# Kernel tuning notes

Hardware: AMD Instinct MI355X
Metric: run time of the kernel (lower is better)

Reference implementation:

```python
import jax, jax.numpy as jnp
import numpy as np

N, E, D, L, R, G, NRXN = 100000, 400000, 256, 3, 4, 2000, 10


def setup_inputs() -> dict:
    key = jax.random.key(0)
    ks = jax.random.split(key, 12)
    s = 1.0 / np.sqrt(D).astype(np.float32)
    return {
        "node_feature": jax.random.normal(ks[0], (N, D), jnp.float32),
        "flag_W": jax.random.normal(ks[1], (2, D), jnp.float32) * s,
        "flag_b": jax.random.normal(ks[2], (D,), jnp.float32) * s,
        "W_self": jax.random.normal(ks[3], (L, D, D), jnp.float32) * s,
        "b_self": jax.random.normal(ks[4], (L, D), jnp.float32) * s,
        "W_rel": jax.random.normal(ks[5], (L, R, D, D), jnp.float32) * s,
        "edge_src": jax.random.randint(ks[6], (E,), 0, N, jnp.int32),
        "edge_dst": jax.random.randint(ks[7], (E,), 0, N, jnp.int32),
        "edge_type": jax.random.randint(ks[8], (E,), 0, R, jnp.int32),
        "batch": jnp.sort(jax.random.randint(ks[9], (N,), 0, G, jnp.int32)),
        "reaction": jax.random.randint(ks[10], (G,), 0, NRXN, jnp.int32),
        "center_mask": jax.random.randint(ks[11], (N,), 0, 2, jnp.int32).astype(bool),
    }


def _rgcn_layer(x, Wself, bself, Wrel, edge_src, edge_dst, edge_type, deg):
    # Relation-wise transform on all nodes [R, N, D], then per-edge gather by
    # (edge_type, src). Masks over edge_type partition edges, so overwriting
    # messages[mask] per relation == selecting the relation's transform per edge.
    h = jnp.einsum('nd,rde->rne', x, Wrel)
    messages = h[edge_type, edge_src]                         # [E, D]
    agg = jax.ops.segment_sum(messages, edge_dst, num_segments=x.shape[0]) / deg
    return jax.nn.relu(x @ Wself + bself + agg)


def reference(node_feature, flag_W, flag_b, W_self, b_self, W_rel,
              edge_src, edge_dst, edge_type, batch, reaction, center_mask):
    n = node_feature.shape[0]
    # flags = [zeros, center_mask]; node_input = node_feature + flag_linear(flags)
    flags = jnp.stack([jnp.zeros((n,), jnp.float32),
                       center_mask.astype(jnp.float32)], axis=-1)  # [N, 2]
    x = node_feature + flags @ flag_W + flag_b
    # degree normalization over destinations (same every layer), clamp min 1
    deg = jnp.maximum(
        jax.ops.segment_sum(jnp.ones((edge_dst.shape[0],), jnp.float32),
                            edge_dst, num_segments=n), 1.0)[:, None]
    hiddens = []
    for l in range(L):
        x = _rgcn_layer(x, W_self[l], b_self[l], W_rel[l],
                        edge_src, edge_dst, edge_type, deg)
        hiddens.append(x)
    node_enc = jnp.concatenate(hiddens, axis=-1)              # [N, L*D]
    # segment mean over graphs
    gsum = jax.ops.segment_sum(node_enc, batch, num_segments=G)
    gcnt = jnp.maximum(
        jax.ops.segment_sum(jnp.ones((n,), jnp.float32), batch, num_segments=G),
        1.0)[:, None]
    graph_feature = gsum / gcnt                               # [G, L*D]
    rxn = jax.nn.one_hot(reaction, NRXN, dtype=jnp.float32)   # [G, NRXN]
    graph_context = jnp.concatenate([graph_feature, rxn], axis=-1)
    node_context = jnp.concatenate(
        [node_enc, node_feature, graph_context[batch]], axis=-1)  # [N, 1802]
    return node_context, graph_context
```

## Files before the change

### kernel.cpp

```cpp
#include <hip/hip_runtime.h>
#include <hip/hip_bf16.h>

typedef _Float16 f16x8 __attribute__((ext_vector_type(8)));
typedef float f32x4 __attribute__((ext_vector_type(4)));

namespace {
constexpr int N_ = 100000;
constexpr int E_ = 400000;
constexpr int D_ = 256;
constexpr int L_ = 3;
constexpr int R_ = 4;
constexpr int G_ = 2000;
constexpr int NRXN_ = 10;
constexpr int CTXW = L_*D_ + D_ + L_*D_ + NRXN_;
constexpr int GCTXW = L_*D_ + NRXN_;
constexpr int NKT = (R_+1)*D_/32;
constexpr int NR = N_*R_;
constexpr int NB2 = (NR + 2047)/2048;
}


__global__ void k_zero(int* __restrict__ p, int n) {
  int i = blockIdx.x*256 + threadIdx.x;
  if (i < n) p[i] = 0;
}

__global__ void k_detect(const unsigned char* __restrict__ cm, int* __restrict__ meta) {
  int tid = threadIdx.x;
  int ok_i = 1, ok_f = 1;
  for (int i = tid; i < 4096; i += 256) {
    unsigned b = cm[i];
    int m = i & 3;
    if (m == 0)      { if (b > 1) ok_i = 0; if (b != 0) ok_f = 0; }
    else if (m == 1) { if (b) { ok_i = 0; ok_f = 0; } }
    else if (m == 2) { if (b) ok_i = 0; if (b != 0 && b != 0x80) ok_f = 0; }
    else             { if (b) ok_i = 0; if (b != 0 && b != 0x3f) ok_f = 0; }
  }
  int all_i = __syncthreads_and(ok_i);
  int all_f = __syncthreads_and(ok_f);
  if (tid == 0) meta[0] = all_i ? 0 : (all_f ? 1 : 2);
}

__global__ void k_hist2(const int* __restrict__ dst, const int* __restrict__ typ,
                        int* __restrict__ hist, int n) {
  int i = blockIdx.x*256 + threadIdx.x;
  if (i < n) atomicAdd(&hist[dst[i]*4 + typ[i]], 1);
}

__global__ void k_hist(const int* __restrict__ key, int* __restrict__ hist, int n) {
  int i = blockIdx.x*256 + threadIdx.x;
  if (i < n) atomicAdd(&hist[key[i]], 1);
}

__global__ void k_scan1(const int* __restrict__ h, int* __restrict__ out,
                        int* __restrict__ bsum, int n) {
  __shared__ int sh[256];
  int t = threadIdx.x;
  int base = blockIdx.x*2048 + t*8;
  int v[8]; int s = 0;
  #pragma unroll
  for (int j = 0; j < 8; ++j) { v[j] = (base+j < n) ? h[base+j] : 0; s += v[j]; }
  sh[t] = s; __syncthreads();
  for (int off = 1; off < 256; off <<= 1) {
    int x = (t >= off) ? sh[t-off] : 0;
    __syncthreads();
    sh[t] += x;
    __syncthreads();
  }
  int ex = sh[t] - s;
  #pragma unroll
  for (int j = 0; j < 8; ++j) { if (base+j < n) out[base+j] = ex; ex += v[j]; }
  if (t == 255) bsum[blockIdx.x] = sh[255];
}

__global__ void k_scan2(int* __restrict__ b, int nb) {
  __shared__ int sh[256];
  int t = threadIdx.x;
  int s = (t < nb) ? b[t] : 0;
  sh[t] = s; __syncthreads();
  for (int off = 1; off < 256; off <<= 1) {
    int x = (t >= off) ? sh[t-off] : 0;
    __syncthreads();
    sh[t] += x;
    __syncthreads();
  }
  if (t < nb) b[t] = sh[t] - s;
}

__global__ void k_scan3(int* __restrict__ eoff, const int* __restrict__ bsum,
                        int* __restrict__ cursor, int n, int total) {
  int i = blockIdx.x*256 + threadIdx.x;
  if (i < n) {
    int v = eoff[i] + bsum[i >> 11];
    eoff[i] = v;
    cursor[i] = v;
  }
  if (i == 0) eoff[n] = total;
}

__global__ void k_scatter2(const int* __restrict__ src, const int* __restrict__ dst,
                           const int* __restrict__ typ, int* __restrict__ cursor,
                           int* __restrict__ out, int n) {
  int i = blockIdx.x*256 + threadIdx.x;
  if (i < n) {
    int key = dst[i]*4 + typ[i];
    int p = atomicAdd(&cursor[key], 1);
    out[p] = src[i];
  }
}

__global__ void k_scan_small(const int* __restrict__ gh, int* __restrict__ goff, int g) {
  __shared__ int sh[256];
  int t = threadIdx.x;
  int v[8]; int s = 0;
  #pragma unroll
  for (int j = 0; j < 8; ++j) { int idx = t*8+j; v[j] = (idx < g) ? gh[idx] : 0; s += v[j]; }
  sh[t] = s; __syncthreads();
  for (int off = 1; off < 256; off <<= 1) {
    int x = (t >= off) ? sh[t-off] : 0;
    __syncthreads();
    sh[t] += x;
    __syncthreads();
  }
  int ex = sh[t] - s;
  #pragma unroll
  for (int j = 0; j < 8; ++j) { int idx = t*8+j; if (idx < g) goff[idx] = ex; ex += v[j]; }
  if (t == 255) goff[g] = sh[255];
}

__global__ void k_pack_w(const float* __restrict__ Wrel, const float* __restrict__ Wself,
                         f16x8* __restrict__ Bp) {
  int id = blockIdx.x*256 + threadIdx.x;
  if (id >= L_*NKT*16*64) return;
  int lane = id & 63; int rest = id >> 6;
  int ct = rest & 15; rest >>= 4;
  int kt = rest % NKT; int l = rest / NKT;
  int q = lane >> 4, ln = lane & 15;
  int col = ct*16 + ln;
  f16x8 o;
  #pragma unroll
  for (int j = 0; j < 8; ++j) {
    int k = kt*32 + q*8 + j;
    float v = (k < R_*D_) ? Wrel[((size_t)l*R_*D_ + k)*D_ + col]
                          : Wself[((size_t)l*D_ + (k - R_*D_))*D_ + col];
    o[j] = (_Float16)v;
  }
  Bp[id] = o;
}

__global__ void k_node_init(const float* __restrict__ nf, const float* __restrict__ fW,
                            const float* __restrict__ fb, const void* __restrict__ cm,
                            const int* __restrict__ meta, _Float16* __restrict__ xa,
                            float* __restrict__ out) {
  int n = blockIdx.x, c = threadIdx.x;
  float v = nf[(size_t)n*D_ + c];
  out[(size_t)n*CTXW + 768 + c] = v;
  int mode = meta[0];
  bool mk;
  if (mode == 0)      mk = ((const int*)cm)[n] != 0;
  else if (mode == 1) mk = ((const float*)cm)[n] != 0.f;
  else                mk = ((const unsigned char*)cm)[n] != 0;
  float x0 = v + (mk ? fW[D_ + c] : 0.f) + fb[c];
  xa[(size_t)n*D_ + c] = (_Float16)x0;
}

__global__ __launch_bounds__(256, 3)
void k_layer(const _Float16* __restrict__ xin, const f16x8* __restrict__ Bp,
             const float* __restrict__ bias, const int* __restrict__ eoff2,
             const int* __restrict__ es, float* __restrict__ outp,
             _Float16* __restrict__ xout) {
  __shared__ f16x8 As16[2][32*32];
  const int tid = threadIdx.x;
  const int lane = tid & 63, wave = tid >> 6;
  const int q = lane >> 4, ln = lane & 15;
  const int m0 = blockIdx.x * 32;
  const int kch = lane & 7;
  const int row = wave*8 + (lane >> 3);
  const int nd  = m0 + row;

  int oo[5];
  #pragma unroll
  for (int j = 0; j < 5; ++j) oo[j] = eoff2[nd*4 + j];
  const int degt = oo[4] - oo[0];
  const float invd = 1.0f / (float)(degt > 1 ? degt : 1);

  f32x4 acc[2][4];
  #pragma unroll
  for (int rt = 0; rt < 2; ++rt)
    #pragma unroll
    for (int cc = 0; cc < 4; ++cc)
      acc[rt][cc] = f32x4{0.f,0.f,0.f,0.f};

  {
    const _Float16* r0 = xin + (size_t)(m0 + ln)*D_;
    const _Float16* r1 = xin + (size_t)(m0 + 16 + ln)*D_;
    #pragma unroll
    for (int kt = 0; kt < 8; ++kt) {
      f16x8 a0 = *(const f16x8*)(r0 + kt*32 + q*8);
      f16x8 a1 = *(const f16x8*)(r1 + kt*32 + q*8);
      f16x8 b[4];
      #pragma unroll
      for (int cc = 0; cc < 4; ++cc)
        b[cc] = Bp[(size_t)((32 + kt)*16 + wave*4 + cc)*64 + lane];
      #pragma unroll
      for (int cc = 0; cc < 4; ++cc) {
        acc[0][cc] = __builtin_amdgcn_mfma_f32_16x16x32_f16(a0, b[cc], acc[0][cc], 0,0,0);
        acc[1][cc] = __builtin_amdgcn_mfma_f32_16x16x32_f16(a1, b[cc], acc[1][cc], 0,0,0);
      }
    }
  }

  #pragma unroll
  for (int r = 0; r < R_; ++r) {
    f32x4 ax[8];
    #pragma unroll
    for (int i = 0; i < 8; ++i) ax[i] = f32x4{0.f,0.f,0.f,0.f};
    for (int e = oo[r]; e < oo[r+1]; ++e) {
      int src = es[e];
      const f16x8* sp = (const f16x8*)(xin + (size_t)src*D_ + kch*32);
      f16x8 w0 = sp[0], w1 = sp[1], w2 = sp[2], w3 = sp[3];
      ax[0] += f32x4{(float)w0[0],(float)w0[1],(float)w0[2],(float)w0[3]};
      ax[1] += f32x4{(float)w0[4],(float)w0[5],(float)w0[6],(float)w0[7]};
      ax[2] += f32x4{(float)w1[0],(float)w1[1],(float)w1[2],(float)w1[3]};
      ax[3] += f32x4{(float)w1[4],(float)w1[5],(float)w1[6],(float)w1[7]};
      ax[4] += f32x4{(float)w2[0],(float)w2[1],(float)w2[2],(float)w2[3]};
      ax[5] += f32x4{(float)w2[4],(float)w2[5],(float)w2[6],(float)w2[7]};
      ax[6] += f32x4{(float)w3[0],(float)w3[1],(float)w3[2],(float)w3[3]};
      ax[7] += f32x4{(float)w3[4],(float)w3[5],(float)w3[6],(float)w3[7]};
    }
    f16x8* dstb = &As16[r & 1][row*32];
    #pragma unroll
    for (int i = 0; i < 4; ++i) {
      f32x4 lo = ax[2*i], hi = ax[2*i+1];
      f16x8 o;
      o[0] = (_Float16)(lo[0]*invd); o[1] = (_Float16)(lo[1]*invd);
      o[2] = (_Float16)(lo[2]*invd); o[3] = (_Float16)(lo[3]*invd);
      o[4] = (_Float16)(hi[0]*invd); o[5] = (_Float16)(hi[1]*invd);
      o[6] = (_Float16)(hi[2]*invd); o[7] = (_Float16)(hi[3]*invd);
      dstb[(kch*4 + i) ^ (row & 7)] = o;
    }
    __syncthreads();
    const f16x8* As = As16[r & 1];
    #pragma unroll
    for (int kt = 0; kt < 8; ++kt) {
      f16x8 a0 = As[(size_t)ln*32      + ((kt*4 + q) ^ (ln & 7))];
      f16x8 a1 = As[(size_t)(16+ln)*32 + ((kt*4 + q) ^ (ln & 7))];
      f16x8 b[4];
      #pragma unroll
      for (int cc = 0; cc < 4; ++cc)
        b[cc] = Bp[(size_t)((r*8 + kt)*16 + wave*4 + cc)*64 + lane];
      #pragma unroll
      for (int cc = 0; cc < 4; ++cc) {
        acc[0][cc] = __builtin_amdgcn_mfma_f32_16x16x32_f16(a0, b[cc], acc[0][cc], 0,0,0);
        acc[1][cc] = __builtin_amdgcn_mfma_f32_16x16x32_f16(a1, b[cc], acc[1][cc], 0,0,0);
      }
    }
  }

  #pragma unroll
  for (int cc = 0; cc < 4; ++cc) {
    int col = (wave*4 + cc)*16 + ln;
    float bv = bias[col];
    #pragma unroll
    for (int rt = 0; rt < 2; ++rt) {
      #pragma unroll
      for (int i = 0; i < 4; ++i) {
        int rrow = m0 + rt*16 + q*4 + i;
        float v = acc[rt][cc][i] + bv;
        v = fmaxf(v, 0.f);
        outp[(size_t)rrow*CTXW + col] = v;
        if (xout) xout[(size_t)rrow*D_ + col] = (_Float16)v;
      }
    }
  }
}

__global__ void k_pool(float* __restrict__ out, const int* __restrict__ goff,
                       const int* __restrict__ rxn) {
  int g = blockIdx.x, t = threadIdx.x;
  int s = goff[g], e = goff[g+1];
  int cnt = e - s;
  float inv = 1.0f / (float)(cnt > 1 ? cnt : 1);
  float a0 = 0.f, a1 = 0.f, a2 = 0.f;
  for (int nn = s; nn < e; ++nn) {
    size_t base = (size_t)nn*CTXW;
    a0 += out[base + t];
    a1 += out[base + 256 + t];
    a2 += out[base + 512 + t];
  }
  size_t gbase = (size_t)N_*CTXW + (size_t)g*GCTXW;
  out[gbase + t]       = a0*inv;
  out[gbase + 256 + t] = a1*inv;
  out[gbase + 512 + t] = a2*inv;
  if (t < NRXN_) out[gbase + 768 + t] = (rxn[g] == t) ? 1.f : 0.f;
}

__global__ void k_bcast(float* __restrict__ out, const int* __restrict__ batch) {
  int nn = blockIdx.x, t = threadIdx.x;
  size_t gbase = (size_t)N_*CTXW + (size_t)batch[nn]*GCTXW;
  size_t nb = (size_t)nn*CTXW + 1024;
  out[nb + t]       = out[gbase + t];
  out[nb + 256 + t] = out[gbase + 256 + t];
  out[nb + 512 + t] = out[gbase + 512 + t];
  if (t < GCTXW - 768) out[nb + 768 + t] = out[gbase + 768 + t];
}

extern "C" void kernel_launch(void* const* d_in, const int* in_sizes, int n_in,
                              void* d_out, int out_size, void* d_ws, size_t ws_size,
                              hipStream_t stream) {
  const float* node_feature = (const float*)d_in[0];
  const float* flag_W  = (const float*)d_in[1];
  const float* flag_b  = (const float*)d_in[2];
  const float* W_self  = (const float*)d_in[3];
  const float* b_self  = (const float*)d_in[4];
  const float* W_rel   = (const float*)d_in[5];
  const int* edge_src  = (const int*)d_in[6];
  const int* edge_dst  = (const int*)d_in[7];
  const int* edge_type = (const int*)d_in[8];
  const int* batch     = (const int*)d_in[9];
  const int* reaction  = (const int*)d_in[10];
  const void* cmask    = d_in[11];
  float* out = (float*)d_out;

  char* ws = (char*)d_ws;
  size_t off = 0;
  auto alloc = [&](size_t bytes) {
    void* p = ws + off;
    off = (off + bytes + 255) & ~(size_t)255;
    return p;
  };
  int* meta          = (int*)alloc(256);
  _Float16* xa       = (_Float16*)alloc((size_t)N_*D_*2);
  _Float16* xb       = (_Float16*)alloc((size_t)N_*D_*2);
  f16x8* Bp          = (f16x8*)alloc((size_t)L_*NKT*16*64*16);
  int* eoff2         = (int*)alloc((size_t)(NR+1)*4);
  int* cursor        = (int*)alloc((size_t)NR*4);
  int* ghist         = (int*)alloc((size_t)G_*4);
  int* goff          = (int*)alloc((size_t)(G_+1)*4);
  int* bsum          = (int*)alloc(1024);
  int* esorted       = (int*)alloc((size_t)E_*4);
  (void)in_sizes; (void)n_in; (void)out_size; (void)ws_size;

  k_detect<<<1, 256, 0, stream>>>((const unsigned char*)cmask, meta);
  k_zero<<<(NR+255)/256, 256, 0, stream>>>(cursor, NR);
  k_zero<<<(G_+255)/256, 256, 0, stream>>>(ghist, G_);
  k_hist2<<<(E_+255)/256, 256, 0, stream>>>(edge_dst, edge_type, cursor, E_);
  k_scan1<<<NB2, 256, 0, stream>>>(cursor, eoff2, bsum, NR);
  k_scan2<<<1, 256, 0, stream>>>(bsum, NB2);
  k_scan3<<<(NR+255)/256, 256, 0, stream>>>(eoff2, bsum, cursor, NR, E_);
  k_scatter2<<<(E_+255)/256, 256, 0, stream>>>(edge_src, edge_dst, edge_type, cursor, esorted, E_);
  k_hist<<<(N_+255)/256, 256, 0, stream>>>(batch, ghist, N_);
  k_scan_small<<<1, 256, 0, stream>>>(ghist, goff, G_);
  k_pack_w<<<(L_*NKT*16*64 + 255)/256, 256, 0, stream>>>(W_rel, W_self, Bp);
  k_node_init<<<N_, 256, 0, stream>>>(node_feature, flag_W, flag_b, cmask, meta, xa, out);

  const int nblk = N_ / 32;
  k_layer<<<nblk, 256, 0, stream>>>(xa, Bp,          b_self,       eoff2, esorted, out,       xb);
  k_layer<<<nblk, 256, 0, stream>>>(xb, Bp + 40960,  b_self + 256, eoff2, esorted, out + 256, xa);
  k_layer<<<nblk, 256, 0, stream>>>(xa, Bp + 81920,  b_self + 512, eoff2, esorted, out + 512, nullptr);

  k_pool<<<G_, 256, 0, stream>>>(out, goff, reaction);
  k_bcast<<<N_, 256, 0, stream>>>(out, batch);
}
```

Measured before the change: 1.561 ms.

## Fuse graph broadcast into pooling, interleave gather loads, raise layer occupancy

The separate broadcast kernel is removed. The pooling kernel now writes the per-graph mean and one-hot directly into each node's context row, which saves a launch and a re-read of graph_context. The edge gather now has the 8 lanes of a row read consecutive 16-byte chunks so accesses coalesce, and the LDS swizzle index is changed to match. The layer kernel's launch bounds rise from 3 to 4 blocks per CU, which may force register spills. Fusing the broadcast into pooling leaves only 2000 blocks, each writing a long serial run of rows, which may cut parallelism for that stage.

```diff
diff --git a/kernel.cpp b/kernel.cpp
--- a/kernel.cpp
+++ b/kernel.cpp
@@ -164,7 +164,7 @@
   xa[(size_t)n*D_ + c] = (_Float16)x0;
 }
 
-__global__ __launch_bounds__(256, 3)
+__global__ __launch_bounds__(256, 4)
 void k_layer(const _Float16* __restrict__ xin, const f16x8* __restrict__ Bp,
              const float* __restrict__ bias, const int* __restrict__ eoff2,
              const int* __restrict__ es, float* __restrict__ outp,
@@ -217,8 +217,11 @@
     for (int i = 0; i < 8; ++i) ax[i] = f32x4{0.f,0.f,0.f,0.f};
     for (int e = oo[r]; e < oo[r+1]; ++e) {
       int src = es[e];
-      const f16x8* sp = (const f16x8*)(xin + (size_t)src*D_ + kch*32);
-      f16x8 w0 = sp[0], w1 = sp[1], w2 = sp[2], w3 = sp[3];
+      const f16x8* sp = (const f16x8*)(xin + (size_t)src*D_);
+      f16x8 w0 = sp[0*8 + kch];
+      f16x8 w1 = sp[1*8 + kch];
+      f16x8 w2 = sp[2*8 + kch];
+      f16x8 w3 = sp[3*8 + kch];
       ax[0] += f32x4{(float)w0[0],(float)w0[1],(float)w0[2],(float)w0[3]};
       ax[1] += f32x4{(float)w0[4],(float)w0[5],(float)w0[6],(float)w0[7]};
       ax[2] += f32x4{(float)w1[0],(float)w1[1],(float)w1[2],(float)w1[3]};
@@ -237,7 +240,7 @@
       o[2] = (_Float16)(lo[2]*invd); o[3] = (_Float16)(lo[3]*invd);
       o[4] = (_Float16)(hi[0]*invd); o[5] = (_Float16)(hi[1]*invd);
       o[6] = (_Float16)(hi[2]*invd); o[7] = (_Float16)(hi[3]*invd);
-      dstb[(kch*4 + i) ^ (row & 7)] = o;
+      dstb[(i*8 + kch) ^ (row & 7)] = o;
     }
     __syncthreads();
     const f16x8* As = As16[r & 1];
@@ -288,21 +291,21 @@
     a1 += out[base + 256 + t];
     a2 += out[base + 512 + t];
   }
+  a0 *= inv; a1 *= inv; a2 *= inv;
+  float rx = 0.f;
+  int rv = rxn[g];
   size_t gbase = (size_t)N_*CTXW + (size_t)g*GCTXW;
-  out[gbase + t]       = a0*inv;
-  out[gbase + 256 + t] = a1*inv;
-  out[gbase + 512 + t] = a2*inv;
-  if (t < NRXN_) out[gbase + 768 + t] = (rxn[g] == t) ? 1.f : 0.f;
-}
-
-__global__ void k_bcast(float* __restrict__ out, const int* __restrict__ batch) {
-  int nn = blockIdx.x, t = threadIdx.x;
-  size_t gbase = (size_t)N_*CTXW + (size_t)batch[nn]*GCTXW;
-  size_t nb = (size_t)nn*CTXW + 1024;
-  out[nb + t]       = out[gbase + t];
-  out[nb + 256 + t] = out[gbase + 256 + t];
-  out[nb + 512 + t] = out[gbase + 512 + t];
-  if (t < GCTXW - 768) out[nb + 768 + t] = out[gbase + 768 + t];
+  out[gbase + t]       = a0;
+  out[gbase + 256 + t] = a1;
+  out[gbase + 512 + t] = a2;
+  if (t < NRXN_) { rx = (rv == t) ? 1.f : 0.f; out[gbase + 768 + t] = rx; }
+  for (int nn = s; nn < e; ++nn) {
+    size_t nb = (size_t)nn*CTXW + 1024;
+    out[nb + t]       = a0;
+    out[nb + 256 + t] = a1;
+    out[nb + 512 + t] = a2;
+    if (t < NRXN_) out[nb + 768 + t] = rx;
+  }
 }
 
 extern "C" void kernel_launch(void* const* d_in, const int* in_sizes, int n_in,
@@ -360,5 +363,4 @@
   k_layer<<<nblk, 256, 0, stream>>>(xa, Bp + 81920,  b_self + 512, eoff2, esorted, out + 512, nullptr);
 
   k_pool<<<G_, 256, 0, stream>>>(out, goff, reaction);
-  k_bcast<<<N_, 256, 0, stream>>>(out, batch);
-}
+}
```

Measured after the change: 1.511 ms. -3.2%, faster.
